# Performance work log

Hardware: AMD Instinct MI355X
Metric: run time of the kernel (lower is better)

Reference implementation:

```python
import jax, jax.numpy as jnp
import numpy as np

B, S, D, R = 8, 2048, 2048, 256


def soft_threshold24(w):
    """2:4 soft-threshold: in each contiguous group of 4 along the last dim,
    keep the top-2 |w| and shrink them by the 3rd-largest |w| (soft threshold),
    zeroing the bottom two. Mirrors soft_threshold24_triton."""
    rows, K = w.shape
    g = w.reshape(rows, K // 4, 4)
    a = jnp.abs(g)
    t = jnp.sort(a, axis=-1)[..., 1:2]  # 2nd smallest == 3rd largest per group
    sp = jnp.sign(g) * jnp.maximum(a - t, 0.0)
    return sp.reshape(rows, K)


def fp16_mm(a, b):
    """fake_fp8_mm: cast operands to fp16, matmul with fp32 accumulation/output."""
    return jnp.matmul(a.astype(jnp.float16), b.astype(jnp.float16),
                      preferred_element_type=jnp.float32)


def sparse_linear(x, w, b, scale):
    """SparseOverlayFunction.forward: 2:4-sparsified, scaled weight + fp16 GEMM."""
    x2 = x.reshape(-1, x.shape[-1])                # [N, K]
    ws = soft_threshold24(w) * scale               # [K, M], 2:4 sparse * learnable scale
    out = fp16_mm(x2, ws)                          # [N, M] fp32
    out = out.reshape(x.shape[:-1] + (w.shape[-1],))
    return out + b


def setup_inputs():
    key = jax.random.key(0)
    ks = jax.random.split(key, 4)
    x = jax.random.normal(ks[0], (B, S, D), jnp.float32)
    weight_in = jax.random.normal(ks[1], (D, R), jnp.float32) * 0.02
    weight_out = jax.random.normal(ks[2], (R, D), jnp.float32) * 0.02
    bias_in = jnp.zeros((R,), jnp.float32)
    bias_out = jax.random.normal(ks[3], (D,), jnp.float32) * 0.01
    sparse_scale_in = jnp.ones((1,), jnp.float32)
    sparse_scale_out = jnp.ones((1,), jnp.float32)
    return {"x": x, "weight_in": weight_in, "weight_out": weight_out,
            "bias_in": bias_in, "bias_out": bias_out,
            "sparse_scale_in": sparse_scale_in, "sparse_scale_out": sparse_scale_out}


def reference(x, weight_in, weight_out, bias_in, bias_out, sparse_scale_in, sparse_scale_out):
    h = sparse_linear(x, weight_in, bias_in, sparse_scale_in)    # [B,S,R]
    y = sparse_linear(h, weight_out, bias_out, sparse_scale_out)  # [B,S,D]
    return y
```

## Files before the change

kernel.cpp:

```cpp
#include <hip/hip_runtime.h>
#include <stdint.h>
#include <stddef.h>

typedef _Float16 f16;
typedef __attribute__((ext_vector_type(8))) _Float16 f16x8;
typedef __attribute__((ext_vector_type(4))) float f32x4;

#define GPTR(p) ((const __attribute__((address_space(1))) void*)(p))
#define LPTR(p) ((__attribute__((address_space(3))) void*)(p))

__device__ __forceinline__ void async16(const void* g, void* l) {
    __builtin_amdgcn_global_load_lds(GPTR(g), LPTR(l), 16, 0, 0);
}

__global__ __launch_bounds__(256) void sparsify_frag(
        const float* __restrict__ W, const float* __restrict__ scale,
        f16* __restrict__ Wf, int K, int M) {
    __shared__ f16 T[64][80];
    const int r0 = blockIdx.y << 6, m0 = blockIdx.x << 6;
    const float s = scale[0];
    const int t = threadIdx.x;
    const int rr = t >> 2, mb = (t & 3) << 4;
    const float* src = W + (size_t)(r0 + rr) * M + m0 + mb;
    #pragma unroll
    for (int j = 0; j < 4; j++) {
        float4 v = *(const float4*)(src + j * 4);
        float a0 = fabsf(v.x), a1 = fabsf(v.y), a2 = fabsf(v.z), a3 = fabsf(v.w);
        float lo1 = fminf(a0, a1), hi1 = fmaxf(a0, a1);
        float lo2 = fminf(a2, a3), hi2 = fmaxf(a2, a3);
        float th = fminf(fmaxf(lo1, lo2), fminf(hi1, hi2));
        int m = mb + j * 4;
        T[m + 0][rr] = (f16)(copysignf(fmaxf(a0 - th, 0.f), v.x) * s);
        T[m + 1][rr] = (f16)(copysignf(fmaxf(a1 - th, 0.f), v.y) * s);
        T[m + 2][rr] = (f16)(copysignf(fmaxf(a2 - th, 0.f), v.z) * s);
        T[m + 3][rr] = (f16)(copysignf(fmaxf(a3 - th, 0.f), v.w) * s);
    }
    __syncthreads();
    const int mm = t >> 2, rb = (t & 3) << 4;
    const int col = m0 + mm;
    const int Mb = M >> 4;
    #pragma unroll
    for (int h = 0; h < 2; h++) {
        int k = r0 + rb + h * 8;
        size_t blk = ((size_t)(k >> 5) * Mb + (col >> 4)) * 64
                   + (size_t)(((k >> 3) & 3) * 16 + (col & 15));
        *(f16x8*)(Wf + blk * 8) = *(const f16x8*)&T[mm][rb + h * 8];
    }
}

__global__ __launch_bounds__(256, 4) void gemm1_kernel(
        const float* __restrict__ A, const f16* __restrict__ Bf,
        const float* __restrict__ bias, f16* __restrict__ Hf) {
    constexpr int K = 2048, BK = 64, NT = K / BK;
    __shared__ f16x8 Ash[512];

    const int tid = threadIdx.x, lane = tid & 63, wv = tid >> 6;
    const int wm = wv & 1, wn = wv >> 1;
    const int lr = lane & 15, q = lane >> 4;

    const int id = blockIdx.x + (blockIdx.y << 2);
    const int xr = id & 7, xt = id >> 3;
    const int nb = xt & 3, p = xr + ((xt >> 2) << 3);
    const int row0 = p << 6, col0 = nb << 6;

    f32x4 acc[2][2] = {};

    const int clr = tid & 15, cq = (tid >> 4) & 3, crg = (tid >> 6) & 3;
    const float* aSrc = A + (size_t)(row0 + crg * 16 + clr) * K + cq * 8;
    constexpr size_t BKT = (size_t)16 * 64 * 8;
    const f16* bBase = Bf + ((size_t)(col0 >> 4) + wn * 2) * 64 * 8 + lane * 8;

    for (int t = 0; t < NT; ++t) {
        const f16* bp = bBase + (size_t)(2 * t) * BKT;
        f16x8 bf[2][2];
        bf[0][0] = *(const f16x8*)(bp);
        bf[0][1] = *(const f16x8*)(bp + 64 * 8);
        bf[1][0] = *(const f16x8*)(bp + BKT);
        bf[1][1] = *(const f16x8*)(bp + BKT + 64 * 8);

        float4 v0 = *(const float4*)(aSrc);
        float4 v1 = *(const float4*)(aSrc + 4);
        float4 v2 = *(const float4*)(aSrc + 32);
        float4 v3 = *(const float4*)(aSrc + 36);
        aSrc += BK;
        f16x8 h0, h1;
        h0[0] = (f16)v0.x; h0[1] = (f16)v0.y; h0[2] = (f16)v0.z; h0[3] = (f16)v0.w;
        h0[4] = (f16)v1.x; h0[5] = (f16)v1.y; h0[6] = (f16)v1.z; h0[7] = (f16)v1.w;
        h1[0] = (f16)v2.x; h1[1] = (f16)v2.y; h1[2] = (f16)v2.z; h1[3] = (f16)v2.w;
        h1[4] = (f16)v3.x; h1[5] = (f16)v3.y; h1[6] = (f16)v3.z; h1[7] = (f16)v3.w;
        Ash[tid]       = h0;
        Ash[tid + 256] = h1;
        __syncthreads();

        #pragma unroll
        for (int ks = 0; ks < 2; ks++) {
            f16x8 af[2];
            af[0] = Ash[(ks * 4 + wm * 2 + 0) * 64 + lane];
            af[1] = Ash[(ks * 4 + wm * 2 + 1) * 64 + lane];
            #pragma unroll
            for (int m = 0; m < 2; m++)
                #pragma unroll
                for (int n = 0; n < 2; n++)
                    acc[m][n] = __builtin_amdgcn_mfma_f32_16x16x32_f16(
                        af[m], bf[ks][n], acc[m][n], 0, 0, 0);
        }
        __syncthreads();
    }

    #pragma unroll
    for (int m = 0; m < 2; m++) {
        int r16 = (row0 + wm * 32 + m * 16) >> 4;
        #pragma unroll
        for (int n = 0; n < 2; n++) {
            int gc = col0 + wn * 32 + n * 16 + lr;
            float bv = bias[gc];
            int kt = gc >> 5, qq = (gc >> 3) & 3, e = gc & 7;
            f16* hb = Hf + ((((size_t)kt * 1024 + r16) * 4 + qq) * 16) * 8 + e;
            #pragma unroll
            for (int rr = 0; rr < 4; rr++)
                hb[(q * 4 + rr) * 8] = (f16)(acc[m][n][rr] + bv);
        }
    }
}

__global__ __launch_bounds__(256, 4) void gemm2_kernel(
        const f16* __restrict__ Hf, const f16* __restrict__ Bf,
        const float* __restrict__ bias, float* __restrict__ Y) {
    constexpr int N = 2048, NT = 4;
    __shared__ f16x8 As[16 * 64];
    __shared__ f16x8 Bs[8 * 64];

    const int tid = threadIdx.x, lane = tid & 63, wv = tid >> 6;
    const int wm = wv & 1, wn = wv >> 1;
    const int lr = lane & 15, q = lane >> 4;

    const int id = blockIdx.x + (blockIdx.y << 5);
    const int xr = id & 7, xt = id >> 3;
    const int bx = xt & 31, by = xr + ((xt >> 5) << 3);
    const int row0 = by << 7, col0 = bx << 6;

    f32x4 acc[4][2] = {};

    for (int t = 0; t < NT; ++t) {
        int kt0 = 2 * t;
        #pragma unroll
        for (int j = 0; j < 4; j++) {
            int i = wv * 4 + j;
            int s = i >> 3, rb = i & 7;
            const f16* srcp = Hf + (((size_t)(kt0 + s) * 1024 + (row0 >> 4) + rb) * 64) * 8
                              + lane * 8;
            async16(srcp, (char*)As + i * 1024);
        }
        #pragma unroll
        for (int j = 0; j < 2; j++) {
            int ch = wv * 2 + j;
            int s = ch >> 2, c = ch & 3;
            const f16* srcp = Bf + (((size_t)(kt0 + s) * 128 + (col0 >> 4) + c) * 64) * 8
                              + lane * 8;
            async16(srcp, (char*)Bs + ch * 1024);
        }
        __syncthreads();
        #pragma unroll
        for (int ks = 0; ks < 2; ks++) {
            f16x8 af[4], bf[2];
            #pragma unroll
            for (int m = 0; m < 4; m++)
                af[m] = As[(ks * 8 + wm * 4 + m) * 64 + lane];
            #pragma unroll
            for (int n = 0; n < 2; n++)
                bf[n] = Bs[(ks * 4 + wn * 2 + n) * 64 + lane];
            #pragma unroll
            for (int m = 0; m < 4; m++)
                #pragma unroll
                for (int n = 0; n < 2; n++)
                    acc[m][n] = __builtin_amdgcn_mfma_f32_16x16x32_f16(
                        af[m], bf[n], acc[m][n], 0, 0, 0);
        }
        __syncthreads();
    }

    #pragma unroll
    for (int m = 0; m < 4; m++) {
        int gr0 = row0 + wm * 64 + m * 16 + q * 4;
        #pragma unroll
        for (int n = 0; n < 2; n++) {
            int gc = col0 + wn * 32 + n * 16 + lr;
            float bv = bias[gc];
            #pragma unroll
            for (int rr = 0; rr < 4; rr++)
                Y[(size_t)(gr0 + rr) * N + gc] = acc[m][n][rr] + bv;
        }
    }
}

extern "C" void kernel_launch(void* const* d_in, const int* in_sizes, int n_in,
                              void* d_out, int out_size, void* d_ws, size_t ws_size,
                              hipStream_t stream) {
    const float* x  = (const float*)d_in[0];
    const float* w1 = (const float*)d_in[1];
    const float* w2 = (const float*)d_in[2];
    const float* b1 = (const float*)d_in[3];
    const float* b2 = (const float*)d_in[4];
    const float* s1 = (const float*)d_in[5];
    const float* s2 = (const float*)d_in[6];
    float* y = (float*)d_out;

    constexpr int NROWS = 8 * 2048;
    constexpr int D = 2048, R = 256;

    char* ws = (char*)d_ws;
    f16* W1f = (f16*)ws;
    f16* W2f = (f16*)(ws + (2u << 20));
    f16* Hf  = (f16*)(ws + (4u << 20));

    hipLaunchKernelGGL(sparsify_frag, dim3(R / 64, D / 64), dim3(256),
                       0, stream, w1, s1, W1f, D, R);
    hipLaunchKernelGGL(sparsify_frag, dim3(D / 64, R / 64), dim3(256),
                       0, stream, w2, s2, W2f, R, D);

    hipLaunchKernelGGL(gemm1_kernel, dim3(4, NROWS / 64), dim3(256),
                       0, stream, x, W1f, b1, Hf);

    hipLaunchKernelGGL(gemm2_kernel, dim3(D / 64, NROWS / 128), dim3(256),
                       0, stream, Hf, W2f, b2, y);
}
```

Measured before the change: 311.5 us.

## Prefetch next K-tile in gemm1 and load gemm2 fragments directly into registers

gemm1 now software-pipelines its loop. The next tile's fp32 activations and fp16 weight fragments are loaded into registers before the MFMAs of the current tile, with sched barriers and an explicit lgkmcnt wait so the global loads stay in flight. gemm2 drops the LDS staging and async loads entirely. Each wave reads its pre-swizzled H and W fragments straight from global memory, with a larger 128x128 tile (4x4 MFMA accumulators per wave), and the grid is halved in x to match. This is meant to hide gemm1's global-load latency and remove gemm2's barriers and LDS traffic, at the cost of more registers and redundant global reads across waves.

```diff
diff --git a/kernel.cpp b/kernel.cpp
--- a/kernel.cpp
+++ b/kernel.cpp
@@ -6,12 +6,7 @@
 typedef __attribute__((ext_vector_type(8))) _Float16 f16x8;
 typedef __attribute__((ext_vector_type(4))) float f32x4;
 
-#define GPTR(p) ((const __attribute__((address_space(1))) void*)(p))
-#define LPTR(p) ((__attribute__((address_space(3))) void*)(p))
-
-__device__ __forceinline__ void async16(const void* g, void* l) {
-    __builtin_amdgcn_global_load_lds(GPTR(g), LPTR(l), 16, 0, 0);
-}
+#define SCHED0() __builtin_amdgcn_sched_barrier(0)
 
 __global__ __launch_bounds__(256) void sparsify_frag(
         const float* __restrict__ W, const float* __restrict__ scale,
@@ -48,6 +43,8 @@
     }
 }
 
+#define MFMA16(a, b, c) __builtin_amdgcn_mfma_f32_16x16x32_f16((a), (b), (c), 0, 0, 0)
+
 __global__ __launch_bounds__(256, 4) void gemm1_kernel(
         const float* __restrict__ A, const f16* __restrict__ Bf,
         const float* __restrict__ bias, f16* __restrict__ Hf) {
@@ -65,46 +62,64 @@
 
     f32x4 acc[2][2] = {};
 
-    const int clr = tid & 15, cq = (tid >> 4) & 3, crg = (tid >> 6) & 3;
+    const int clr = tid & 15, cq = (tid >> 4) & 3, crg = tid >> 6;
     const float* aSrc = A + (size_t)(row0 + crg * 16 + clr) * K + cq * 8;
-    constexpr size_t BKT = (size_t)16 * 64 * 8;
-    const f16* bBase = Bf + ((size_t)(col0 >> 4) + wn * 2) * 64 * 8 + lane * 8;
+    const f16* bBase = Bf + ((size_t)(col0 >> 4) + wn * 2) * 512 + lane * 8;
+
+    float4 a0 = *(const float4*)(aSrc);
+    float4 a1 = *(const float4*)(aSrc + 4);
+    float4 a2 = *(const float4*)(aSrc + 32);
+    float4 a3 = *(const float4*)(aSrc + 36);
+    f16x8 bA = *(const f16x8*)(bBase);
+    f16x8 bB = *(const f16x8*)(bBase + 512);
+    f16x8 bC = *(const f16x8*)(bBase + 8192);
+    f16x8 bD = *(const f16x8*)(bBase + 8192 + 512);
 
     for (int t = 0; t < NT; ++t) {
-        const f16* bp = bBase + (size_t)(2 * t) * BKT;
-        f16x8 bf[2][2];
-        bf[0][0] = *(const f16x8*)(bp);
-        bf[0][1] = *(const f16x8*)(bp + 64 * 8);
-        bf[1][0] = *(const f16x8*)(bp + BKT);
-        bf[1][1] = *(const f16x8*)(bp + BKT + 64 * 8);
-
-        float4 v0 = *(const float4*)(aSrc);
-        float4 v1 = *(const float4*)(aSrc + 4);
-        float4 v2 = *(const float4*)(aSrc + 32);
-        float4 v3 = *(const float4*)(aSrc + 36);
-        aSrc += BK;
         f16x8 h0, h1;
-        h0[0] = (f16)v0.x; h0[1] = (f16)v0.y; h0[2] = (f16)v0.z; h0[3] = (f16)v0.w;
-        h0[4] = (f16)v1.x; h0[5] = (f16)v1.y; h0[6] = (f16)v1.z; h0[7] = (f16)v1.w;
-        h1[0] = (f16)v2.x; h1[1] = (f16)v2.y; h1[2] = (f16)v2.z; h1[3] = (f16)v2.w;
-        h1[4] = (f16)v3.x; h1[5] = (f16)v3.y; h1[6] = (f16)v3.z; h1[7] = (f16)v3.w;
+        h0[0] = (f16)a0.x; h0[1] = (f16)a0.y; h0[2] = (f16)a0.z; h0[3] = (f16)a0.w;
+        h0[4] = (f16)a1.x; h0[5] = (f16)a1.y; h0[6] = (f16)a1.z; h0[7] = (f16)a1.w;
+        h1[0] = (f16)a2.x; h1[1] = (f16)a2.y; h1[2] = (f16)a2.z; h1[3] = (f16)a2.w;
+        h1[4] = (f16)a3.x; h1[5] = (f16)a3.y; h1[6] = (f16)a3.z; h1[7] = (f16)a3.w;
         Ash[tid]       = h0;
         Ash[tid + 256] = h1;
-        __syncthreads();
-
-        #pragma unroll
-        for (int ks = 0; ks < 2; ks++) {
-            f16x8 af[2];
-            af[0] = Ash[(ks * 4 + wm * 2 + 0) * 64 + lane];
-            af[1] = Ash[(ks * 4 + wm * 2 + 1) * 64 + lane];
-            #pragma unroll
-            for (int m = 0; m < 2; m++)
-                #pragma unroll
-                for (int n = 0; n < 2; n++)
-                    acc[m][n] = __builtin_amdgcn_mfma_f32_16x16x32_f16(
-                        af[m], bf[ks][n], acc[m][n], 0, 0, 0);
-        }
-        __syncthreads();
+
+        const int tn = (t + 1 < NT) ? t + 1 : NT - 1;
+        const float* ap = aSrc + (size_t)tn * BK;
+        float4 n0 = *(const float4*)(ap);
+        float4 n1 = *(const float4*)(ap + 4);
+        float4 n2 = *(const float4*)(ap + 32);
+        float4 n3 = *(const float4*)(ap + 36);
+        const f16* bp = bBase + (size_t)(2 * tn) * 8192;
+        f16x8 nA = *(const f16x8*)(bp);
+        f16x8 nB = *(const f16x8*)(bp + 512);
+        f16x8 nC = *(const f16x8*)(bp + 8192);
+        f16x8 nD = *(const f16x8*)(bp + 8192 + 512);
+
+        SCHED0();
+        asm volatile("s_waitcnt lgkmcnt(0)" ::: "memory");
+        __builtin_amdgcn_s_barrier();
+        SCHED0();
+
+        f16x8 af00 = Ash[(wm * 2 + 0) * 64 + lane];
+        f16x8 af01 = Ash[(wm * 2 + 1) * 64 + lane];
+        f16x8 af10 = Ash[256 + (wm * 2 + 0) * 64 + lane];
+        f16x8 af11 = Ash[256 + (wm * 2 + 1) * 64 + lane];
+        acc[0][0] = MFMA16(af00, bA, acc[0][0]);
+        acc[0][1] = MFMA16(af00, bB, acc[0][1]);
+        acc[1][0] = MFMA16(af01, bA, acc[1][0]);
+        acc[1][1] = MFMA16(af01, bB, acc[1][1]);
+        acc[0][0] = MFMA16(af10, bC, acc[0][0]);
+        acc[0][1] = MFMA16(af10, bD, acc[0][1]);
+        acc[1][0] = MFMA16(af11, bC, acc[1][0]);
+        acc[1][1] = MFMA16(af11, bD, acc[1][1]);
+
+        SCHED0();
+        __builtin_amdgcn_s_barrier();
+        SCHED0();
+
+        a0 = n0; a1 = n1; a2 = n2; a3 = n3;
+        bA = nA; bB = nB; bC = nC; bD = nD;
     }
 
     #pragma unroll
@@ -126,65 +141,45 @@
 __global__ __launch_bounds__(256, 4) void gemm2_kernel(
         const f16* __restrict__ Hf, const f16* __restrict__ Bf,
         const float* __restrict__ bias, float* __restrict__ Y) {
-    constexpr int N = 2048, NT = 4;
-    __shared__ f16x8 As[16 * 64];
-    __shared__ f16x8 Bs[8 * 64];
-
+    constexpr int N = 2048;
     const int tid = threadIdx.x, lane = tid & 63, wv = tid >> 6;
     const int wm = wv & 1, wn = wv >> 1;
     const int lr = lane & 15, q = lane >> 4;
 
-    const int id = blockIdx.x + (blockIdx.y << 5);
+    const int id = blockIdx.x + (blockIdx.y << 4);
     const int xr = id & 7, xt = id >> 3;
-    const int bx = xt & 31, by = xr + ((xt >> 5) << 3);
-    const int row0 = by << 7, col0 = bx << 6;
-
-    f32x4 acc[4][2] = {};
-
-    for (int t = 0; t < NT; ++t) {
-        int kt0 = 2 * t;
-        #pragma unroll
-        for (int j = 0; j < 4; j++) {
-            int i = wv * 4 + j;
-            int s = i >> 3, rb = i & 7;
-            const f16* srcp = Hf + (((size_t)(kt0 + s) * 1024 + (row0 >> 4) + rb) * 64) * 8
-                              + lane * 8;
-            async16(srcp, (char*)As + i * 1024);
-        }
-        #pragma unroll
-        for (int j = 0; j < 2; j++) {
-            int ch = wv * 2 + j;
-            int s = ch >> 2, c = ch & 3;
-            const f16* srcp = Bf + (((size_t)(kt0 + s) * 128 + (col0 >> 4) + c) * 64) * 8
-                              + lane * 8;
-            async16(srcp, (char*)Bs + ch * 1024);
-        }
-        __syncthreads();
-        #pragma unroll
-        for (int ks = 0; ks < 2; ks++) {
-            f16x8 af[4], bf[2];
+    const int bx = xt & 15, by = xr + ((xt >> 4) << 3);
+    const int row0 = by << 7, col0 = bx << 7;
+
+    f32x4 acc[4][4] = {};
+
+    const size_t r16b = (size_t)(row0 >> 4) + wm * 4;
+    const size_t c16b = (size_t)(col0 >> 4) + wn * 4;
+
+    #pragma unroll
+    for (int kt = 0; kt < 8; kt++) {
+        f16x8 af[4], bf[4];
+        #pragma unroll
+        for (int m = 0; m < 4; m++)
+            af[m] = *(const f16x8*)(Hf + ((size_t)kt * 1024 + r16b + m) * 512
+                                    + lane * 8);
+        #pragma unroll
+        for (int n = 0; n < 4; n++)
+            bf[n] = *(const f16x8*)(Bf + ((size_t)kt * 128 + c16b + n) * 512
+                                    + lane * 8);
+        #pragma unroll
+        for (int m = 0; m < 4; m++)
             #pragma unroll
-            for (int m = 0; m < 4; m++)
-                af[m] = As[(ks * 8 + wm * 4 + m) * 64 + lane];
-            #pragma unroll
-            for (int n = 0; n < 2; n++)
-                bf[n] = Bs[(ks * 4 + wn * 2 + n) * 64 + lane];
-            #pragma unroll
-            for (int m = 0; m < 4; m++)
-                #pragma unroll
-                for (int n = 0; n < 2; n++)
-                    acc[m][n] = __builtin_amdgcn_mfma_f32_16x16x32_f16(
-                        af[m], bf[n], acc[m][n], 0, 0, 0);
-        }
-        __syncthreads();
+            for (int n = 0; n < 4; n++)
+                acc[m][n] = MFMA16(af[m], bf[n], acc[m][n]);
     }
 
     #pragma unroll
     for (int m = 0; m < 4; m++) {
         int gr0 = row0 + wm * 64 + m * 16 + q * 4;
         #pragma unroll
-        for (int n = 0; n < 2; n++) {
-            int gc = col0 + wn * 32 + n * 16 + lr;
+        for (int n = 0; n < 4; n++) {
+            int gc = col0 + wn * 64 + n * 16 + lr;
             float bv = bias[gc];
             #pragma unroll
             for (int rr = 0; rr < 4; rr++)
@@ -221,6 +216,6 @@
     hipLaunchKernelGGL(gemm1_kernel, dim3(4, NROWS / 64), dim3(256),
                        0, stream, x, W1f, b1, Hf);
 
-    hipLaunchKernelGGL(gemm2_kernel, dim3(D / 64, NROWS / 128), dim3(256),
+    hipLaunchKernelGGL(gemm2_kernel, dim3(D / 128, NROWS / 128), dim3(256),
                        0, stream, Hf, W2f, b2, y);
 }
```

New measurement: 313.5 us. No clear change (+0.6%).
